# Kernel tuning notes

Measured on AMD Instinct MI355X. Metric: run time of the kernel, lower is better.

## Reference

```python
import jax, jax.numpy as jnp
import numpy as np

B, X, Y, Z, C = 2, 128, 128, 128, 4
OX, OY, OZ = 96, 96, 96

def setup_inputs() -> dict:
    key = jax.random.key(0)
    k1, k2 = jax.random.split(key)
    inputs = jax.random.normal(k1, (B, X, Y, Z, C), dtype=jnp.float32)
    # sample coordinates roughly spanning the input volume (can go slightly
    # out of range; REPLICATE boundary clamps indices)
    sample_coords = jax.random.uniform(
        k2, (B, OX, OY, OZ, 3), dtype=jnp.float32,
        minval=-1.0, maxval=float(X))
    return {"inputs": inputs, "sample_coords": sample_coords}

def reference(inputs, sample_coords):
    # Trilinear resampling with REPLICATE boundary (NiftyNet ResamplerLayer,
    # interpolation='LINEAR', boundary='REPLICATE').
    sizes = inputs.shape[1:-1]                      # (X, Y, Z)
    base = jnp.floor(sample_coords)                 # [B, ox, oy, oz, 3]
    w0 = sample_coords - base                       # fractional weight (non-ZERO boundary)
    w1 = 1.0 - w0
    # REPLICATE boundary: clamp floor/ceil indices into [0, size-1]
    fl = [jnp.clip(base[..., d], 0, sizes[d] - 1).astype(jnp.int32) for d in range(3)]
    cl = [jnp.clip(base[..., d] + 1.0, 0, sizes[d] - 1).astype(jnp.int32) for d in range(3)]
    bidx = jnp.arange(inputs.shape[0]).reshape(-1, 1, 1, 1)  # batch ids, broadcast
    out = jnp.zeros(sample_coords.shape[:-1] + (inputs.shape[-1],), inputs.dtype)
    # 8 corner gathers; bc[d]==1 -> ceil index with fractional weight w0[d]
    for i in range(8):
        bc = [(i >> (2 - d)) & 1 for d in range(3)]
        cx, cy, cz = (cl[d] if bc[d] else fl[d] for d in range(3))
        w = (w0[..., 0] if bc[0] else w1[..., 0]) \
            * (w0[..., 1] if bc[1] else w1[..., 1]) \
            * (w0[..., 2] if bc[2] else w1[..., 2])
        out = out + inputs[bidx, cx, cy, cz] * w[..., None]
    return out
```

## Files before the change

kernel.cpp:

```cpp
#include <hip/hip_runtime.h>

constexpr int B  = 2;
constexpr int X  = 128, Y = 128, Z = 128, C = 4;
constexpr int OX = 96,  OY = 96,  OZ = 96;
constexpr int NPTS = B * OX * OY * OZ;
constexpr int PTS_PER_BATCH = OX * OY * OZ;

constexpr int NBINS   = 4096;
constexpr int BIN_CAP = 768;
constexpr int RX = 9, RY = 9, RZ = 17;
constexpr int REG3 = RX * RY * RZ;

constexpr size_t REC_BYTES = (size_t)NBINS * BIN_CAP * 16;
constexpr size_t CUR_OFF   = REC_BYTES;
constexpr size_t WS_NEEDED = CUR_OFF + (size_t)NBINS * 4;

__device__ __forceinline__ int point_bin(float cx, float cy, float cz, int b) {
    const int x = min(max((int)floorf(cx), 0), X - 1) >> 3;
    const int y = min(max((int)floorf(cy), 0), Y - 1) >> 3;
    const int z = min(max((int)floorf(cz), 0), Z - 1) >> 4;
    return (b << 11) + (x << 7) + (y << 3) + z;
}

constexpr int SC_THREADS = 1024;
constexpr int SC_PPT     = 8;
constexpr int SC_PPB     = SC_THREADS * SC_PPT;
constexpr int SC_NBLK    = NPTS / SC_PPB;

__global__ __launch_bounds__(SC_THREADS) void scatter_kernel(
    const float* __restrict__ coords, int* __restrict__ cursors,
    float4* __restrict__ records)
{
    __shared__ int h[NBINS];
    const int t = threadIdx.x;
    const int blkBase = blockIdx.x * SC_PPB;

    #pragma unroll
    for (int j = 0; j < 4; ++j) h[t + j * 1024] = 0;
    __syncthreads();

    int   bins[SC_PPT];
    float pcx[SC_PPT], pcy[SC_PPT], pcz[SC_PPT];
    #pragma unroll
    for (int p = 0; p < SC_PPT; ++p) {
        const int idx = blkBase + p * SC_THREADS + t;
        pcx[p] = coords[(size_t)idx * 3 + 0];
        pcy[p] = coords[(size_t)idx * 3 + 1];
        pcz[p] = coords[(size_t)idx * 3 + 2];
        const int b = idx / PTS_PER_BATCH;
        bins[p] = point_bin(pcx[p], pcy[p], pcz[p], b);
        atomicAdd(&h[bins[p]], 1);
    }
    __syncthreads();

    #pragma unroll
    for (int j = 0; j < 4; ++j) {
        const int bi = t + j * 1024;
        const int cnt = h[bi];
        h[bi] = cnt ? (bi * BIN_CAP + atomicAdd(&cursors[bi], cnt)) : 0;
    }
    __syncthreads();

    #pragma unroll
    for (int p = 0; p < SC_PPT; ++p) {
        const int idx = blkBase + p * SC_THREADS + t;
        const int pos = atomicAdd(&h[bins[p]], 1);
        records[pos] = make_float4(pcx[p], pcy[p], pcz[p], __int_as_float(idx));
    }
}

constexpr int NXCD = 8;
constexpr int K4_CPX = NBINS / NXCD;

__global__ __launch_bounds__(512) void cell_kernel(
    const float* __restrict__ inp, const float4* __restrict__ records,
    const int* __restrict__ cursors, float4* __restrict__ out)
{
    const int pb = blockIdx.x;
    const int bin = (pb & (NXCD - 1)) * K4_CPX + (pb >> 3);

    const int b  = bin >> 11;
    const int cx = (bin >> 7) & 15;
    const int cy = (bin >> 3) & 15;
    const int cz = bin & 7;
    const int bx = cx << 3, by = cy << 3, bz = cz << 4;

    __shared__ float4 tile[REG3];

    const float4* in4 = (const float4*)inp + (size_t)b * X * Y * Z;
    for (int i = threadIdx.x; i < REG3; i += 512) {
        const int lx = i / (RY * RZ);
        const int r  = i % (RY * RZ);
        const int ly = r / RZ;
        const int lz = r % RZ;
        const int gx = min(bx + lx, X - 1);
        const int gy = min(by + ly, Y - 1);
        const int gz = min(bz + lz, Z - 1);
        tile[i] = in4[(gx * Y + gy) * Z + gz];
    }
    __syncthreads();

    const int start = bin * BIN_CAP;
    const int cnt   = cursors[bin];

    for (int k = threadIdx.x; k < cnt; k += 512) {
        const float4 rec = records[start + k];
        const float pcx = rec.x, pcy = rec.y, pcz = rec.z;
        const int ptid = __float_as_int(rec.w);

        const float fx = floorf(pcx), fy = floorf(pcy), fz = floorf(pcz);
        const float wx0 = pcx - fx, wy0 = pcy - fy, wz0 = pcz - fz;
        const float wx1 = 1.0f - wx0, wy1 = 1.0f - wy0, wz1 = 1.0f - wz0;

        const int x0 = (int)fminf(fmaxf(fx,        0.0f), (float)(X - 1)) - bx;
        const int x1 = (int)fminf(fmaxf(fx + 1.0f, 0.0f), (float)(X - 1)) - bx;
        const int y0 = (int)fminf(fmaxf(fy,        0.0f), (float)(Y - 1)) - by;
        const int y1 = (int)fminf(fmaxf(fy + 1.0f, 0.0f), (float)(Y - 1)) - by;
        const int z0 = (int)fminf(fmaxf(fz,        0.0f), (float)(Z - 1)) - bz;
        const int z1 = (int)fminf(fmaxf(fz + 1.0f, 0.0f), (float)(Z - 1)) - bz;

        const int xo0 = x0 * (RY * RZ), xo1 = x1 * (RY * RZ);
        const int yo0 = y0 * RZ,        yo1 = y1 * RZ;

        const float4 v000 = tile[xo0 + yo0 + z0];
        const float4 v001 = tile[xo0 + yo0 + z1];
        const float4 v010 = tile[xo0 + yo1 + z0];
        const float4 v011 = tile[xo0 + yo1 + z1];
        const float4 v100 = tile[xo1 + yo0 + z0];
        const float4 v101 = tile[xo1 + yo0 + z1];
        const float4 v110 = tile[xo1 + yo1 + z0];
        const float4 v111 = tile[xo1 + yo1 + z1];

        float4 r;
        #define LERP4(a, b_, wA, wB, dst)                  \
            dst.x = (a).x * (wA) + (b_).x * (wB);          \
            dst.y = (a).y * (wA) + (b_).y * (wB);          \
            dst.z = (a).z * (wA) + (b_).z * (wB);          \
            dst.w = (a).w * (wA) + (b_).w * (wB);
        float4 c00, c01, c10, c11, c0, c1;
        LERP4(v000, v001, wz1, wz0, c00);
        LERP4(v010, v011, wz1, wz0, c01);
        LERP4(v100, v101, wz1, wz0, c10);
        LERP4(v110, v111, wz1, wz0, c11);
        LERP4(c00, c01, wy1, wy0, c0);
        LERP4(c10, c11, wy1, wy0, c1);
        LERP4(c0, c1, wx1, wx0, r);
        #undef LERP4

        out[ptid] = r;
    }
}

__global__ __launch_bounds__(256) void resampler_direct_kernel(
    const float* __restrict__ inp, const float* __restrict__ coords,
    float4* __restrict__ out)
{
    const int tid = blockIdx.x * blockDim.x + threadIdx.x;
    if (tid >= NPTS) return;
    const int b = tid / PTS_PER_BATCH;
    const float cx = coords[(size_t)tid * 3 + 0];
    const float cy = coords[(size_t)tid * 3 + 1];
    const float cz = coords[(size_t)tid * 3 + 2];
    const float bx = floorf(cx), by = floorf(cy), bz = floorf(cz);
    const float wx0 = cx - bx, wy0 = cy - by, wz0 = cz - bz;
    const float wx1 = 1.0f - wx0, wy1 = 1.0f - wy0, wz1 = 1.0f - wz0;
    const int x0 = (int)fminf(fmaxf(bx,        0.0f), (float)(X - 1));
    const int x1 = (int)fminf(fmaxf(bx + 1.0f, 0.0f), (float)(X - 1));
    const int y0 = (int)fminf(fmaxf(by,        0.0f), (float)(Y - 1));
    const int y1 = (int)fminf(fmaxf(by + 1.0f, 0.0f), (float)(Y - 1));
    const int z0 = (int)fminf(fmaxf(bz,        0.0f), (float)(Z - 1));
    const int z1 = (int)fminf(fmaxf(bz + 1.0f, 0.0f), (float)(Z - 1));
    const float4* in4 = (const float4*)inp + (size_t)b * X * Y * Z;
    const int xo0 = x0 * (Y * Z), xo1 = x1 * (Y * Z);
    const int yo0 = y0 * Z,       yo1 = y1 * Z;
    const float4 v000 = in4[xo0 + yo0 + z0];
    const float4 v001 = in4[xo0 + yo0 + z1];
    const float4 v010 = in4[xo0 + yo1 + z0];
    const float4 v011 = in4[xo0 + yo1 + z1];
    const float4 v100 = in4[xo1 + yo0 + z0];
    const float4 v101 = in4[xo1 + yo0 + z1];
    const float4 v110 = in4[xo1 + yo1 + z0];
    const float4 v111 = in4[xo1 + yo1 + z1];
    float4 r;
    #define LERP4(a, b_, wA, wB, dst)                  \
        dst.x = (a).x * (wA) + (b_).x * (wB);          \
        dst.y = (a).y * (wA) + (b_).y * (wB);          \
        dst.z = (a).z * (wA) + (b_).z * (wB);          \
        dst.w = (a).w * (wA) + (b_).w * (wB);
    float4 c00, c01, c10, c11, c0, c1;
    LERP4(v000, v001, wz1, wz0, c00);
    LERP4(v010, v011, wz1, wz0, c01);
    LERP4(v100, v101, wz1, wz0, c10);
    LERP4(v110, v111, wz1, wz0, c11);
    LERP4(c00, c01, wy1, wy0, c0);
    LERP4(c10, c11, wy1, wy0, c1);
    LERP4(c0, c1, wx1, wx0, r);
    #undef LERP4
    out[tid] = r;
}

extern "C" void kernel_launch(void* const* d_in, const int* in_sizes, int n_in,
                              void* d_out, int out_size, void* d_ws, size_t ws_size,
                              hipStream_t stream) {
    const float* inp    = (const float*)d_in[0];
    const float* coords = (const float*)d_in[1];
    float4* out = (float4*)d_out;

    if (ws_size < WS_NEEDED) {
        const int blocks = (NPTS + 255) / 256;
        resampler_direct_kernel<<<blocks, 256, 0, stream>>>(inp, coords, out);
        return;
    }

    char* ws = (char*)d_ws;
    float4* records = (float4*)ws;
    int* cursors = (int*)(ws + CUR_OFF);

    hipMemsetAsync(cursors, 0, NBINS * sizeof(int), stream);
    scatter_kernel<<<SC_NBLK, SC_THREADS, 0, stream>>>(coords, cursors, records);
    cell_kernel<<<NBINS, 512, 0, stream>>>(inp, records, cursors, out);
}
```

Before: 69.52 us.

## Batch tile loads in registers, process two points per thread, halve cell block size

The cell kernel now runs 256 threads per block. Each thread first loads all of its halo-tile elements into registers, then writes them to shared memory, so the global loads can overlap instead of alternating load and store. The point loop handles two records per iteration to raise memory-level parallelism, and the per-bin count is clamped to the bin capacity. The scatter kernel processes 16 points per thread instead of 8, which halves the scatter grid and increases register pressure.

```diff
diff --git a/kernel.cpp b/kernel.cpp
--- a/kernel.cpp
+++ b/kernel.cpp
@@ -23,7 +23,7 @@
 }
 
 constexpr int SC_THREADS = 1024;
-constexpr int SC_PPT     = 8;
+constexpr int SC_PPT     = 16;
 constexpr int SC_PPB     = SC_THREADS * SC_PPT;
 constexpr int SC_NBLK    = NPTS / SC_PPB;
 
@@ -71,8 +71,10 @@
 
 constexpr int NXCD = 8;
 constexpr int K4_CPX = NBINS / NXCD;
-
-__global__ __launch_bounds__(512) void cell_kernel(
+constexpr int CT = 256;
+constexpr int ST_N = (REG3 + CT - 1) / CT;
+
+__global__ __launch_bounds__(CT) void cell_kernel(
     const float* __restrict__ inp, const float4* __restrict__ records,
     const int* __restrict__ cursors, float4* __restrict__ out)
 {
@@ -88,7 +90,11 @@
     __shared__ float4 tile[REG3];
 
     const float4* in4 = (const float4*)inp + (size_t)b * X * Y * Z;
-    for (int i = threadIdx.x; i < REG3; i += 512) {
+
+    float4 st[ST_N];
+    #pragma unroll
+    for (int j = 0; j < ST_N; ++j) {
+        const int i = min(threadIdx.x + j * CT, REG3 - 1);
         const int lx = i / (RY * RZ);
         const int r  = i % (RY * RZ);
         const int ly = r / RZ;
@@ -96,59 +102,72 @@
         const int gx = min(bx + lx, X - 1);
         const int gy = min(by + ly, Y - 1);
         const int gz = min(bz + lz, Z - 1);
-        tile[i] = in4[(gx * Y + gy) * Z + gz];
+        st[j] = in4[(gx * Y + gy) * Z + gz];
+    }
+    #pragma unroll
+    for (int j = 0; j < ST_N; ++j) {
+        const int i = min(threadIdx.x + j * CT, REG3 - 1);
+        tile[i] = st[j];
     }
     __syncthreads();
 
     const int start = bin * BIN_CAP;
-    const int cnt   = cursors[bin];
-
-    for (int k = threadIdx.x; k < cnt; k += 512) {
-        const float4 rec = records[start + k];
-        const float pcx = rec.x, pcy = rec.y, pcz = rec.z;
-        const int ptid = __float_as_int(rec.w);
-
-        const float fx = floorf(pcx), fy = floorf(pcy), fz = floorf(pcz);
-        const float wx0 = pcx - fx, wy0 = pcy - fy, wz0 = pcz - fz;
-        const float wx1 = 1.0f - wx0, wy1 = 1.0f - wy0, wz1 = 1.0f - wz0;
-
-        const int x0 = (int)fminf(fmaxf(fx,        0.0f), (float)(X - 1)) - bx;
-        const int x1 = (int)fminf(fmaxf(fx + 1.0f, 0.0f), (float)(X - 1)) - bx;
-        const int y0 = (int)fminf(fmaxf(fy,        0.0f), (float)(Y - 1)) - by;
-        const int y1 = (int)fminf(fmaxf(fy + 1.0f, 0.0f), (float)(Y - 1)) - by;
-        const int z0 = (int)fminf(fmaxf(fz,        0.0f), (float)(Z - 1)) - bz;
-        const int z1 = (int)fminf(fmaxf(fz + 1.0f, 0.0f), (float)(Z - 1)) - bz;
-
-        const int xo0 = x0 * (RY * RZ), xo1 = x1 * (RY * RZ);
-        const int yo0 = y0 * RZ,        yo1 = y1 * RZ;
-
-        const float4 v000 = tile[xo0 + yo0 + z0];
-        const float4 v001 = tile[xo0 + yo0 + z1];
-        const float4 v010 = tile[xo0 + yo1 + z0];
-        const float4 v011 = tile[xo0 + yo1 + z1];
-        const float4 v100 = tile[xo1 + yo0 + z0];
-        const float4 v101 = tile[xo1 + yo0 + z1];
-        const float4 v110 = tile[xo1 + yo1 + z0];
-        const float4 v111 = tile[xo1 + yo1 + z1];
-
-        float4 r;
-        #define LERP4(a, b_, wA, wB, dst)                  \
-            dst.x = (a).x * (wA) + (b_).x * (wB);          \
-            dst.y = (a).y * (wA) + (b_).y * (wB);          \
-            dst.z = (a).z * (wA) + (b_).z * (wB);          \
-            dst.w = (a).w * (wA) + (b_).w * (wB);
-        float4 c00, c01, c10, c11, c0, c1;
-        LERP4(v000, v001, wz1, wz0, c00);
-        LERP4(v010, v011, wz1, wz0, c01);
-        LERP4(v100, v101, wz1, wz0, c10);
-        LERP4(v110, v111, wz1, wz0, c11);
-        LERP4(c00, c01, wy1, wy0, c0);
-        LERP4(c10, c11, wy1, wy0, c1);
-        LERP4(c0, c1, wx1, wx0, r);
-        #undef LERP4
-
-        out[ptid] = r;
-    }
+    const int cnt   = min(cursors[bin], BIN_CAP);
+
+    #define COMPUTE_PT(rec, rdst)                                             \
+    {                                                                         \
+        const float pcx = rec.x, pcy = rec.y, pcz = rec.z;                    \
+        const float fx = floorf(pcx), fy = floorf(pcy), fz = floorf(pcz);     \
+        const float wx0 = pcx - fx, wy0 = pcy - fy, wz0 = pcz - fz;           \
+        const float wx1 = 1.0f - wx0, wy1 = 1.0f - wy0, wz1 = 1.0f - wz0;     \
+        const int x0 = (int)fminf(fmaxf(fx,        0.0f), (float)(X-1)) - bx; \
+        const int x1 = (int)fminf(fmaxf(fx + 1.0f, 0.0f), (float)(X-1)) - bx; \
+        const int y0 = (int)fminf(fmaxf(fy,        0.0f), (float)(Y-1)) - by; \
+        const int y1 = (int)fminf(fmaxf(fy + 1.0f, 0.0f), (float)(Y-1)) - by; \
+        const int z0 = (int)fminf(fmaxf(fz,        0.0f), (float)(Z-1)) - bz; \
+        const int z1 = (int)fminf(fmaxf(fz + 1.0f, 0.0f), (float)(Z-1)) - bz; \
+        const int xo0 = x0 * (RY * RZ), xo1 = x1 * (RY * RZ);                 \
+        const int yo0 = y0 * RZ,        yo1 = y1 * RZ;                        \
+        const float4 v000 = tile[xo0 + yo0 + z0];                             \
+        const float4 v001 = tile[xo0 + yo0 + z1];                             \
+        const float4 v010 = tile[xo0 + yo1 + z0];                             \
+        const float4 v011 = tile[xo0 + yo1 + z1];                             \
+        const float4 v100 = tile[xo1 + yo0 + z0];                             \
+        const float4 v101 = tile[xo1 + yo0 + z1];                             \
+        const float4 v110 = tile[xo1 + yo1 + z0];                             \
+        const float4 v111 = tile[xo1 + yo1 + z1];                             \
+        float4 c00, c01, c10, c11, c0, c1;                                    \
+        LERP4(v000, v001, wz1, wz0, c00);                                     \
+        LERP4(v010, v011, wz1, wz0, c01);                                     \
+        LERP4(v100, v101, wz1, wz0, c10);                                     \
+        LERP4(v110, v111, wz1, wz0, c11);                                     \
+        LERP4(c00, c01, wy1, wy0, c0);                                        \
+        LERP4(c10, c11, wy1, wy0, c1);                                        \
+        LERP4(c0, c1, wx1, wx0, rdst);                                        \
+    }
+    #define LERP4(a, b_, wA, wB, dst)                  \
+        dst.x = (a).x * (wA) + (b_).x * (wB);          \
+        dst.y = (a).y * (wA) + (b_).y * (wB);          \
+        dst.z = (a).z * (wA) + (b_).z * (wB);          \
+        dst.w = (a).w * (wA) + (b_).w * (wB);
+
+    for (int k0 = threadIdx.x; k0 < cnt; k0 += 2 * CT) {
+        const int k1 = k0 + CT;
+        const bool hasB = (k1 < cnt);
+        const float4 recA = records[start + k0];
+        const float4 recB = records[start + (hasB ? k1 : k0)];
+        const int tidA = __float_as_int(recA.w);
+        const int tidB = __float_as_int(recB.w);
+
+        float4 rA, rB;
+        COMPUTE_PT(recA, rA);
+        COMPUTE_PT(recB, rB);
+
+        out[tidA] = rA;
+        if (hasB) out[tidB] = rB;
+    }
+    #undef COMPUTE_PT
+    #undef LERP4
 }
 
 __global__ __launch_bounds__(256) void resampler_direct_kernel(
@@ -218,5 +237,5 @@
 
     hipMemsetAsync(cursors, 0, NBINS * sizeof(int), stream);
     scatter_kernel<<<SC_NBLK, SC_THREADS, 0, stream>>>(coords, cursors, records);
-    cell_kernel<<<NBINS, 512, 0, stream>>>(inp, records, cursors, out);
-}
+    cell_kernel<<<NBINS, CT, 0, stream>>>(inp, records, cursors, out);
+}
```

Result: no change. 68.50 us (-1.5%).
